# Performance work log

Measured on AMD Instinct MI355X. Metric: run time of the kernel, lower is better.

Reference implementation:

```python
import jax, jax.numpy as jnp
import numpy as np

BN_EPS = 1e-3


def _knn_group(p1, p2, k):
    # p1, p2: [B, N, 3]. For each point in p1, find k nearest in p2.
    d2 = (jnp.sum(p1 * p1, -1)[:, :, None]
          + jnp.sum(p2 * p2, -1)[:, None, :]
          - 2.0 * jnp.einsum('bnd,bmd->bnm', p1, p2))  # [B,N,N]
    _, idx = jax.lax.top_k(-d2, k)                      # [B,N,k]
    nn = jax.vmap(lambda pts, ind: pts[ind])(p2, idx)   # [B,N,k,3]
    resi = nn - p1[:, :, None, :]                       # [B,N,k,3]
    ss = jnp.sum(resi * resi, -1, keepdims=True)
    dist = jnp.sqrt(jnp.maximum(ss, 1e-12))             # safe norm
    feat = jnp.concatenate([resi, dist], -1)            # [B,N,k,4]
    return feat.transpose(0, 3, 1, 2), nn.transpose(0, 3, 1, 2)  # [B,4,N,k],[B,3,N,k]


def _conv_bn_relu(x, W, b, g, be, m, v):
    # 1x1 conv over channel dim: x [B,C,N,K], W [O,C]
    x = jnp.einsum('bcnk,oc->bonk', x, W) + b[None, :, None, None]
    x = (x - m[None, :, None, None]) * (g / jnp.sqrt(v + BN_EPS))[None, :, None, None] + be[None, :, None, None]
    return jax.nn.relu(x)


def setup_inputs() -> dict:
    key = jax.random.key(0)
    ks = jax.random.split(key, 20)
    B, N = 8, 2048
    chans = [4, 64, 64, 128]
    inp = {
        'points1': jax.random.normal(ks[0], (B, 3, N), jnp.float32),
        'points2': jax.random.normal(ks[1], (B, 3, N), jnp.float32),
    }
    for i in range(3):
        ci, co = chans[i], chans[i + 1]
        base = 2 + i * 6
        scale = 1.0 / np.sqrt(ci)
        inp[f'W{i+1}'] = jax.random.uniform(ks[base], (co, ci), jnp.float32, -scale, scale)
        inp[f'b{i+1}'] = jax.random.uniform(ks[base + 1], (co,), jnp.float32, -scale, scale)
        inp[f'g{i+1}'] = 1.0 + 0.1 * jax.random.normal(ks[base + 2], (co,), jnp.float32)
        inp[f'be{i+1}'] = 0.1 * jax.random.normal(ks[base + 3], (co,), jnp.float32)
        inp[f'm{i+1}'] = 0.05 * jax.random.normal(ks[base + 4], (co,), jnp.float32)
        inp[f'v{i+1}'] = jax.random.uniform(ks[base + 5], (co,), jnp.float32, 0.5, 1.5)
    inp['k'] = 32
    inp['t'] = 1
    return inp


def reference(points1, points2, W1, b1, g1, be1, m1, v1, W2, b2, g2, be2, m2, v2,
              W3, b3, g3, be3, m3, v3, k, t):
    p1 = points1.transpose(0, 2, 1)  # [B,N,3]
    p2 = points2.transpose(0, 2, 1)
    f1, nn1 = _knn_group(p1, p1, k)
    f2, nn2 = _knn_group(p1, p2, k)
    feats = jnp.concatenate([f1, f2], -1)          # [B,4,N,2k]
    grouped = jnp.concatenate([nn1, nn2], -1)      # [B,3,N,2k]
    x = _conv_bn_relu(feats, W1, b1, g1, be1, m1, v1)
    x = _conv_bn_relu(x, W2, b2, g2, be2, m2, v2)
    x = _conv_bn_relu(x, W3, b3, g3, be3, m3, v3)
    x = jnp.max(x, axis=1)                         # [B,N,2k] max over channels
    w = jax.nn.softmax(x, axis=-1)                 # softmax over 2k neighbors
    fused = jnp.sum(w[:, None, :, :] * grouped, -1)  # [B,3,N]
    return fused
```

## Files before the change

### kernel.cpp

```cpp
#include <hip/hip_runtime.h>
#include <hip/hip_bf16.h>
#include <stdint.h>

#define BB 8
#define NN 2048

#define OFF_B1 272
#define OFF_B2 4432
#define OFF_B3 12688
#define IDX_BYTE_OFF 65536
#define T_BASE   (65536 + 2*1024*1024)
#define T1_OFF   T_BASE
#define T2H_OFF  (T1_OFF + 4096)
#define T2L_OFF  (T2H_OFF + 9216)
#define T3H_OFF  (T2L_OFF + 9216)
#define T3L_OFF  (T3H_OFF + 18432)
#define L_T1   0
#define L_T2H  2048
#define L_T2L  6656
#define L_T3H  11264
#define L_T3L  20480
#define L_HALVES 29696

typedef __attribute__((ext_vector_type(4))) float f32x4;
typedef __attribute__((ext_vector_type(8))) short s16x8;

__device__ __forceinline__ float ldany(const void* p, long i, int isf32) {
    if (isf32) return ((const float*)p)[i];
    uint32_t u = ((uint32_t)((const uint16_t*)p)[i]) << 16;
    float f; __builtin_memcpy(&f, &u, 4); return f;
}
__device__ __forceinline__ uint16_t f2bf(float f) {
    uint32_t u; __builtin_memcpy(&u, &f, 4);
    return (uint16_t)((u + 0x7FFFu + ((u >> 16) & 1u)) >> 16);
}
__device__ __forceinline__ float bf2f(uint16_t h) {
    uint32_t u = ((uint32_t)h) << 16;
    float f; __builtin_memcpy(&f, &u, 4); return f;
}
__device__ __forceinline__ uint32_t pk2(float a, float b) {
    __hip_bfloat162 h = __float22bfloat162_rn(make_float2(a, b));
    uint32_t u; __builtin_memcpy(&u, &h, 4); return u;
}
__device__ __forceinline__ s16x8 mk8(uint32_t a, uint32_t b, uint32_t c, uint32_t d) {
    uint32_t t[4] = {a, b, c, d}; s16x8 r; __builtin_memcpy(&r, t, 16); return r;
}
__device__ __forceinline__ float sane(float v) {
    return (v == v && v > -1e30f && v < 1e30f) ? v : 0.f;
}
__device__ __forceinline__ int kperm_pos(int kk) {
    int g = kk >> 5, c5 = kk & 31;
    int sub = (c5 >> 4) & 1, q = (c5 >> 2) & 3, r = c5 & 3;
    return 32 * g + 8 * q + 4 * sub + r;
}

__global__ void k0_fold(const void* p1,
                        const void* W1, const void* b1, const void* g1, const void* be1, const void* m1, const void* v1,
                        const void* W2, const void* b2, const void* g2, const void* be2, const void* m2, const void* v2,
                        const void* W3, const void* b3, const void* g3, const void* be3, const void* m3, const void* v3,
                        float* wsf, int* wsi) {
    __shared__ int s_cnt;
    int t = threadIdx.x;
    if (t == 0) s_cnt = 0;
    __syncthreads();
    const uint16_t* u = (const uint16_t*)p1;
    int c = 0;
    for (int i = t; i < 4096; i += 256) {
        uint16_t x = u[i];
        uint32_t e = (x >> 7) & 0xFF;
        c += ((e >= 0x70 && e <= 0x84) || x == 0) ? 1 : 0;
    }
    atomicAdd(&s_cnt, c);
    __syncthreads();
    int isf32 = (s_cnt < 3686) ? 1 : 0;
    if (blockIdx.x == 0 && t == 0) wsi[0] = isf32;

    uint16_t* t1  = (uint16_t*)((char*)wsf + T1_OFF);
    uint16_t* t2h = (uint16_t*)((char*)wsf + T2H_OFF);
    uint16_t* t2l = (uint16_t*)((char*)wsf + T2L_OFF);
    uint16_t* t3h = (uint16_t*)((char*)wsf + T3H_OFF);
    uint16_t* t3l = (uint16_t*)((char*)wsf + T3L_OFF);

    int gid = blockIdx.x * 256 + t;
    if (gid < 4096) {
        int o = gid >> 6, kk = gid & 63;
        float s = ldany(g2, o, isf32) * rsqrtf(ldany(v2, o, isf32) + 1e-3f);
        float w = ldany(W2, gid, isf32) * s;
        uint16_t wh = f2bf(w);
        int pos = o * 72 + kperm_pos(kk);
        t2h[pos] = wh; t2l[pos] = f2bf(w - bf2f(wh));
    } else if (gid < 12288) {
        int e = gid - 4096;
        int o = e >> 6, kk = e & 63;
        float s = ldany(g3, o, isf32) * rsqrtf(ldany(v3, o, isf32) + 1e-3f);
        float w = ldany(W3, e, isf32) * s;
        uint16_t wh = f2bf(w);
        int pos = o * 72 + kperm_pos(kk);
        t3h[pos] = wh; t3l[pos] = f2bf(w - bf2f(wh));
    } else if (gid < 12544) {
        int e = gid - 12288;
        int co = e >> 2, cc = e & 3;
        float s = ldany(g1, co, isf32) * rsqrtf(ldany(v1, co, isf32) + 1e-3f);
        float w = ldany(W1, co*4 + cc, isf32) * s;
        uint16_t wh = f2bf(w), wl = f2bf(w - bf2f(wh));
        t1[co*32 + cc]     = wh;
        t1[co*32 + 4 + cc] = wh;
        t1[co*32 + 8 + cc] = wl;
    } else if (gid < 13824) {
        int e = gid - 12544;
        int co = e / 20, k = e - co * 20;
        t1[co*32 + 12 + k] = 0;
    } else if (gid < 13888) {
        int o = gid - 13824;
        float s = ldany(g1, o, isf32) * rsqrtf(ldany(v1, o, isf32) + 1e-3f);
        wsf[OFF_B1 + o] = (ldany(b1, o, isf32) - ldany(m1, o, isf32)) * s + ldany(be1, o, isf32);
    } else if (gid < 13952) {
        int o = gid - 13888;
        float s = ldany(g2, o, isf32) * rsqrtf(ldany(v2, o, isf32) + 1e-3f);
        wsf[OFF_B2 + o] = (ldany(b2, o, isf32) - ldany(m2, o, isf32)) * s + ldany(be2, o, isf32);
    } else if (gid < 14080) {
        int o = gid - 13952;
        float s = ldany(g3, o, isf32) * rsqrtf(ldany(v3, o, isf32) + 1e-3f);
        wsf[OFF_B3 + o] = (ldany(b3, o, isf32) - ldany(m3, o, isf32)) * s + ldany(be3, o, isf32);
    }
}

__launch_bounds__(256)
__global__ void k1_knn(const void* p1, const void* p2, const int* wsi, uint16_t* idxout) {
    __shared__ unsigned long long smem[4 * 128];

    int isf32 = wsi[0];
    int lane = threadIdx.x & 63;
    int wave = threadIdx.x >> 6;
    int qidx = blockIdx.x * 4 + wave;
    int b = qidx >> 11, n = qidx & 2047;
    long base = (long)b * 3 * NN;

    float qx = ldany(p1, base + n,        isf32);
    float qy = ldany(p1, base + NN + n,   isf32);
    float qz = ldany(p1, base + 2*NN + n, isf32);
    float s1 = qx * qx + qy * qy + qz * qz;

    uint32_t kbA[32], kbB[32];
    if (!isf32) {
        const uint16_t* u1 = (const uint16_t*)p1 + base;
        const uint16_t* u2 = (const uint16_t*)p2 + base;
        #pragma unroll
        for (int tgt = 0; tgt < 2; tgt++) {
            const uint16_t* tpu = tgt ? u2 : u1;
            uint32_t* kb = tgt ? kbB : kbA;
            const uint4* rx = (const uint4*)(tpu);
            const uint4* ry = (const uint4*)(tpu + NN);
            const uint4* rz = (const uint4*)(tpu + 2*NN);
            #pragma unroll
            for (int i = 0; i < 4; i++) {
                int v4 = i * 64 + lane;
                uint4 X = rx[v4], Y = ry[v4], Z = rz[v4];
                uint32_t xw[4] = {X.x, X.y, X.z, X.w};
                uint32_t yw[4] = {Y.x, Y.y, Y.z, Y.w};
                uint32_t zw[4] = {Z.x, Z.y, Z.z, Z.w};
                #pragma unroll
                for (int j = 0; j < 4; j++) {
                    #pragma unroll
                    for (int w = 0; w < 2; w++) {
                        uint32_t ux = (w == 0) ? (xw[j] << 16) : (xw[j] & 0xFFFF0000u);
                        uint32_t uy = (w == 0) ? (yw[j] << 16) : (yw[j] & 0xFFFF0000u);
                        uint32_t uz = (w == 0) ? (zw[j] << 16) : (zw[j] & 0xFFFF0000u);
                        float nx, ny, nz;
                        __builtin_memcpy(&nx, &ux, 4); __builtin_memcpy(&ny, &uy, 4); __builtin_memcpy(&nz, &uz, 4);
                        float s2  = nx * nx + ny * ny + nz * nz;
                        float dot = qx * nx + qy * ny + qz * nz;
                        float d2  = fmaxf((s1 + s2) - 2.0f * dot, 0.0f);
                        uint32_t bits; __builtin_memcpy(&bits, &d2, 4);
                        kb[i*8 + j*2 + w] = bits;
                    }
                }
            }
        }
    } else {
        #pragma unroll
        for (int i = 0; i < 32; i++) {
            int j = i * 64 + lane;
            float ax = ldany(p1, base + j,        isf32);
            float ay = ldany(p1, base + NN + j,   isf32);
            float az = ldany(p1, base + 2*NN + j, isf32);
            float d2a = fmaxf((s1 + ax*ax + ay*ay + az*az) - 2.0f*(qx*ax + qy*ay + qz*az), 0.0f);
            uint32_t ba; __builtin_memcpy(&ba, &d2a, 4);
            kbA[i] = ba;
            float bx = ldany(p2, base + j,        isf32);
            float by = ldany(p2, base + NN + j,   isf32);
            float bz = ldany(p2, base + 2*NN + j, isf32);
            float d2b = fmaxf((s1 + bx*bx + by*by + bz*bz) - 2.0f*(qx*bx + qy*by + qz*bz), 0.0f);
            uint32_t bb; __builtin_memcpy(&bb, &d2b, 4);
            kbB[i] = bb;
        }
    }

    uint32_t loA = 0u, hiA = 0x7F800001u, tauA = 0u;
    uint32_t loB = 0u, hiB = 0x7F800001u, tauB = 0u;
    int cpA = -1, cpB = -1;
    bool dA = false, dB = false;
    while (!(dA && dB)) {
        uint32_t midA = dA ? tauA : (loA + ((hiA - loA) >> 1));
        uint32_t midB = dB ? tauB : (loB + ((hiB - loB) >> 1));
        int cA = 0, cB = 0;
        #pragma unroll
        for (int i = 0; i < 32; i++) {
            cA += (kbA[i] < midA) ? 1 : 0;
            cB += (kbB[i] < midB) ? 1 : 0;
        }
        uint32_t pk = (uint32_t)cA | ((uint32_t)cB << 16);
        #pragma unroll
        for (int m = 1; m < 64; m <<= 1) pk += (uint32_t)__shfl_xor((int)pk, m, 64);
        int totA = (int)(pk & 0xFFFFu);
        int totB = (int)(pk >> 16);
        if (!dA) {
            if (totA < 32)      loA = midA;
            else if (totA > 64) hiA = midA;
            else { tauA = midA; cpA = cA; dA = true; }
            if (!dA && hiA - loA <= 1u) { tauA = hiA; dA = true; }
        }
        if (!dB) {
            if (totB < 32)      loB = midB;
            else if (totB > 64) hiB = midB;
            else { tauB = midB; cpB = cB; dB = true; }
            if (!dB && hiB - loB <= 1u) { tauB = hiB; dB = true; }
        }
    }
    if (cpA < 0) {
        int c2 = 0;
        #pragma unroll
        for (int i = 0; i < 32; i++) c2 += (kbA[i] < tauA) ? 1 : 0;
        cpA = c2;
    }
    if (cpB < 0) {
        int c2 = 0;
        #pragma unroll
        for (int i = 0; i < 32; i++) c2 += (kbB[i] < tauB) ? 1 : 0;
        cpB = c2;
    }

    uint32_t pc = (uint32_t)cpA | ((uint32_t)cpB << 16);
    uint32_t off = pc;
    #pragma unroll
    for (int d = 1; d < 64; d <<= 1) {
        uint32_t y = (uint32_t)__shfl_up((int)off, d, 64);
        if (lane >= d) off += y;
    }
    off -= pc;
    int oA = (int)(off & 0xFFFFu);
    int oB = (int)(off >> 16);

    unsigned long long* slA = smem + wave * 128;
    unsigned long long* slB = slA + 64;
    slA[lane] = ~0ull;
    slB[lane] = ~0ull;
    __syncthreads();
    #pragma unroll
    for (int s = 0; s < 32; s++) {
        unsigned idxv = isf32 ? (unsigned)(s * 64 + lane)
                              : (unsigned)((s >> 3) * 512 + 8 * lane + (s & 7));
        if (kbA[s] < tauA && oA < 64) {
            slA[oA] = (((unsigned long long)kbA[s]) << 32) | idxv;
            oA++;
        }
        if (kbB[s] < tauB && oB < 64) {
            slB[oB] = (((unsigned long long)kbB[s]) << 32) | idxv;
            oB++;
        }
    }
    __syncthreads();
    unsigned long long keyA = slA[lane];
    unsigned long long keyB = slB[lane];

    #pragma unroll
    for (int sz = 2; sz <= 64; sz <<= 1) {
        #pragma unroll
        for (int st = sz >> 1; st > 0; st >>= 1) {
            bool up    = ((lane & sz) == 0);
            bool lower = ((lane & st) == 0);
            unsigned long long otA = __shfl_xor(keyA, st, 64);
            unsigned long long otB = __shfl_xor(keyB, st, 64);
            unsigned long long mnA = (keyA < otA) ? keyA : otA;
            unsigned long long mxA = (keyA < otA) ? otA : keyA;
            keyA = (lower == up) ? mnA : mxA;
            unsigned long long mnB = (keyB < otB) ? keyB : otB;
            unsigned long long mxB = (keyB < otB) ? otB : keyB;
            keyB = (lower == up) ? mnB : mxB;
        }
    }

    if (lane < 32) {
        long obase = ((long)qidx) << 6;
        idxout[obase + lane]      = (uint16_t)(keyA & 0x7FFu);
        idxout[obase + 32 + lane] = (uint16_t)(keyB & 0x7FFu);
    }
}

__launch_bounds__(256)
__global__ void k2_mlp(const void* p1, const void* p2, const float* __restrict__ wsf, const int* wsi,
                       const uint16_t* __restrict__ idxin, void* outp) {
    __shared__ uint4 shw4[L_HALVES / 8];

    {
        const uint4* src = (const uint4*)((const char*)wsf + T1_OFF);
        for (int i = threadIdx.x; i < L_HALVES / 8; i += 256) shw4[i] = src[i];
    }
    __syncthreads();
    const uint16_t* shw = (const uint16_t*)shw4;
    const uint16_t* T1  = shw + L_T1;
    const uint16_t* T2H = shw + L_T2H;
    const uint16_t* T2L = shw + L_T2L;
    const uint16_t* T3H = shw + L_T3H;
    const uint16_t* T3L = shw + L_T3L;

    int isf32 = wsi[0];
    int lane = threadIdx.x & 63;
    int wave = threadIdx.x >> 6;
    int c = lane & 15;
    int q = lane >> 4;
    int qidx = blockIdx.x * 4 + wave;
    int b = qidx >> 11, n = qidx & 2047;
    long base = (long)b * 3 * NN;

    float qx = sane(ldany(p1, base + n,        isf32));
    float qy = sane(ldany(p1, base + NN + n,   isf32));
    float qz = sane(ldany(p1, base + 2*NN + n, isf32));

    int idx = idxin[((long)qidx << 6) + lane] & 2047;
    const void* sp = (lane < 32) ? p1 : p2;
    float nx = sane(ldany(sp, base + idx,        isf32));
    float ny = sane(ldany(sp, base + NN + idx,   isf32));
    float nz = sane(ldany(sp, base + 2*NN + idx, isf32));

    float r0 = nx - qx, r1 = ny - qy, r2 = nz - qz;
    float ss = fmaf(r0, r0, fmaf(r1, r1, r2 * r2));
    float dist = sqrtf(fmaxf(ss, 1e-12f));

    const float* B1 = wsf + OFF_B1;
    const float* B2 = wsf + OFF_B2;
    const float* B3 = wsf + OFF_B3;

    s16x8 b1f[4];
    #pragma unroll
    for (int nt = 0; nt < 4; nt++) {
        int src = 16 * nt + c;
        float f0 = __shfl(r0, src, 64);
        float f1 = __shfl(r1, src, 64);
        float f2v = __shfl(r2, src, 64);
        float f3v = __shfl(dist, src, 64);
        uint16_t h0 = f2bf(f0), h1 = f2bf(f1), h2 = f2bf(f2v), h3 = f2bf(f3v);
        uint16_t l0 = f2bf(f0 - bf2f(h0)), l1 = f2bf(f1 - bf2f(h1));
        uint16_t l2 = f2bf(f2v - bf2f(h2)), l3 = f2bf(f3v - bf2f(h3));
        s16x8 v;
        bool qa = (q < 2);
        bool qb = (q == 0);
        v[0] = qa ? (short)h0 : (short)0;
        v[1] = qa ? (short)h1 : (short)0;
        v[2] = qa ? (short)h2 : (short)0;
        v[3] = qa ? (short)h3 : (short)0;
        v[4] = qb ? (short)l0 : (short)0;
        v[5] = qb ? (short)l1 : (short)0;
        v[6] = qb ? (short)l2 : (short)0;
        v[7] = qb ? (short)l3 : (short)0;
        b1f[nt] = v;
    }

    f32x4 d1[4][4];
    #pragma unroll
    for (int mt = 0; mt < 4; mt++) {
        s16x8 a1 = *(const s16x8*)(T1 + (16 * mt + c) * 32 + q * 8);
        f32x4 bias = *(const f32x4*)(B1 + 16 * mt + 4 * q);
        #pragma unroll
        for (int nt = 0; nt < 4; nt++) {
            d1[mt][nt] = __builtin_amdgcn_mfma_f32_16x16x32_bf16(a1, b1f[nt], bias, 0, 0, 0);
        }
    }

    auto mkfrag = [](const f32x4& dlo, const f32x4& dhi) -> s16x8 {
        return mk8(pk2(fmaxf(dlo[0], 0.f), fmaxf(dlo[1], 0.f)),
                   pk2(fmaxf(dlo[2], 0.f), fmaxf(dlo[3], 0.f)),
                   pk2(fmaxf(dhi[0], 0.f), fmaxf(dhi[1], 0.f)),
                   pk2(fmaxf(dhi[2], 0.f), fmaxf(dhi[3], 0.f)));
    };

    f32x4 d2[4][4];
    #pragma unroll
    for (int mt = 0; mt < 4; mt++) {
        f32x4 bias = *(const f32x4*)(B2 + 16 * mt + 4 * q);
        #pragma unroll
        for (int nt = 0; nt < 4; nt++) d2[mt][nt] = bias;
    }
    #pragma unroll
    for (int g = 0; g < 2; g++) {
        s16x8 fh[4];
        #pragma unroll
        for (int nt = 0; nt < 4; nt++) fh[nt] = mkfrag(d1[2*g][nt], d1[2*g+1][nt]);
        #pragma unroll
        for (int mt = 0; mt < 4; mt++) {
            s16x8 ah = *(const s16x8*)(T2H + (16 * mt + c) * 72 + 32 * g + 8 * q);
            s16x8 al = *(const s16x8*)(T2L + (16 * mt + c) * 72 + 32 * g + 8 * q);
            #pragma unroll
            for (int nt = 0; nt < 4; nt++) {
                f32x4 acc = d2[mt][nt];
                acc = __builtin_amdgcn_mfma_f32_16x16x32_bf16(ah, fh[nt], acc, 0, 0, 0);
                acc = __builtin_amdgcn_mfma_f32_16x16x32_bf16(al, fh[nt], acc, 0, 0, 0);
                d2[mt][nt] = acc;
            }
        }
    }

    s16x8 f3h[2][4];
    #pragma unroll
    for (int g = 0; g < 2; g++)
        #pragma unroll
        for (int nt = 0; nt < 4; nt++) f3h[g][nt] = mkfrag(d2[2*g][nt], d2[2*g+1][nt]);

    float mx[4] = {-1e30f, -1e30f, -1e30f, -1e30f};
    #pragma unroll
    for (int mt = 0; mt < 8; mt++) {
        f32x4 bias = *(const f32x4*)(B3 + 16 * mt + 4 * q);
        f32x4 acc[4];
        #pragma unroll
        for (int nt = 0; nt < 4; nt++) acc[nt] = bias;
        #pragma unroll
        for (int g = 0; g < 2; g++) {
            s16x8 ah = *(const s16x8*)(T3H + (16 * mt + c) * 72 + 32 * g + 8 * q);
            s16x8 al = *(const s16x8*)(T3L + (16 * mt + c) * 72 + 32 * g + 8 * q);
            #pragma unroll
            for (int nt = 0; nt < 4; nt++) {
                f32x4 a = acc[nt];
                a = __builtin_amdgcn_mfma_f32_16x16x32_bf16(ah, f3h[g][nt], a, 0, 0, 0);
                a = __builtin_amdgcn_mfma_f32_16x16x32_bf16(al, f3h[g][nt], a, 0, 0, 0);
                acc[nt] = a;
            }
        }
        #pragma unroll
        for (int nt = 0; nt < 4; nt++) {
            mx[nt] = fmaxf(mx[nt], fmaxf(fmaxf(acc[nt][0], acc[nt][1]), fmaxf(acc[nt][2], acc[nt][3])));
        }
    }

    #pragma unroll
    for (int nt = 0; nt < 4; nt++) {
        mx[nt] = fmaxf(mx[nt], __shfl_xor(mx[nt], 16, 64));
        mx[nt] = fmaxf(mx[nt], __shfl_xor(mx[nt], 32, 64));
        mx[nt] = fmaxf(mx[nt], 0.f);
    }
    float mall = fmaxf(fmaxf(mx[0], mx[1]), fmaxf(mx[2], mx[3]));
    #pragma unroll
    for (int m = 1; m < 16; m <<= 1) mall = fmaxf(mall, __shfl_xor(mall, m, 64));
    float e0 = __expf(mx[0] - mall), e1 = __expf(mx[1] - mall);
    float e2 = __expf(mx[2] - mall), e3 = __expf(mx[3] - mall);
    float s = e0 + e1 + e2 + e3;
    #pragma unroll
    for (int m = 1; m < 16; m <<= 1) s += __shfl_xor(s, m, 64);
    float eown = (q == 0) ? e0 : (q == 1) ? e1 : (q == 2) ? e2 : e3;
    float w = eown / s;

    float sx = w * nx, sy = w * ny, sz = w * nz;
    #pragma unroll
    for (int m = 1; m < 64; m <<= 1) {
        sx += __shfl_xor(sx, m, 64);
        sy += __shfl_xor(sy, m, 64);
        sz += __shfl_xor(sz, m, 64);
    }

    if (lane < 3) {
        float v = (lane == 0) ? sx : ((lane == 1) ? sy : sz);
        long oi = base + (long)lane * NN + n;
        if (isf32) {
            ((float*)outp)[oi] = v;
        } else {
            ((uint16_t*)outp)[oi] = f2bf(v);
        }
    }
}

extern "C" void kernel_launch(void* const* d_in, const int* in_sizes, int n_in,
                              void* d_out, int out_size, void* d_ws, size_t ws_size,
                              hipStream_t stream) {
    const void* p1 = d_in[0];
    const void* p2 = d_in[1];
    float* wsf = (float*)d_ws;
    int*   wsi = (int*)d_ws;
    uint16_t* idxbuf = (uint16_t*)((char*)d_ws + IDX_BYTE_OFF);

    k0_fold<<<64, 256, 0, stream>>>(p1,
        d_in[2],  d_in[3],  d_in[4],  d_in[5],  d_in[6],  d_in[7],
        d_in[8],  d_in[9],  d_in[10], d_in[11], d_in[12], d_in[13],
        d_in[14], d_in[15], d_in[16], d_in[17], d_in[18], d_in[19],
        wsf, wsi);

    k1_knn<<<(BB * NN) / 4, 256, 0, stream>>>(p1, p2, wsi, idxbuf);

    k2_mlp<<<(BB * NN) / 4, 256, 0, stream>>>(p1, p2, wsf, wsi, idxbuf, d_out);
}
```

Measured before the change: 278.7 us.

## Replace kNN bitonic sort with exact radix-select threshold and ballot compaction

The kNN kernel now binary-searches the distance bit pattern for an exact 32nd-smallest threshold, counting with wave ballots and popcounts instead of per-lane counts plus shuffle reductions. Ties are broken by a second binary search over index. Selected indices are written straight to global memory through ballot/mbcnt compaction, which removes the LDS staging, both __syncthreads and the 64-element bitonic sort. The output order changes from distance-sorted to scan order, which is harmless because the downstream softmax-weighted sum does not depend on order. Occupancy is also hinted with launch_bounds(256,4), and the search now costs more iterations because it must hit exactly 32 rather than any count in 32..64.

Result: slower. 303.8 us (+9.0%).

```diff
diff --git a/kernel.cpp b/kernel.cpp
--- a/kernel.cpp
+++ b/kernel.cpp
@@ -47,6 +47,10 @@
 }
 __device__ __forceinline__ float sane(float v) {
     return (v == v && v > -1e30f && v < 1e30f) ? v : 0.f;
+}
+__device__ __forceinline__ int mbcnt64(unsigned long long m) {
+    return __builtin_amdgcn_mbcnt_hi((uint32_t)(m >> 32),
+           __builtin_amdgcn_mbcnt_lo((uint32_t)m, 0));
 }
 __device__ __forceinline__ int kperm_pos(int kk) {
     int g = kk >> 5, c5 = kk & 31;
@@ -125,10 +129,8 @@
     }
 }
 
-__launch_bounds__(256)
+__launch_bounds__(256, 4)
 __global__ void k1_knn(const void* p1, const void* p2, const int* wsi, uint16_t* idxout) {
-    __shared__ unsigned long long smem[4 * 128];
-
     int isf32 = wsi[0];
     int lane = threadIdx.x & 63;
     int wave = threadIdx.x >> 6;
@@ -196,104 +198,108 @@
         }
     }
 
-    uint32_t loA = 0u, hiA = 0x7F800001u, tauA = 0u;
-    uint32_t loB = 0u, hiB = 0x7F800001u, tauB = 0u;
-    int cpA = -1, cpB = -1;
-    bool dA = false, dB = false;
-    while (!(dA && dB)) {
-        uint32_t midA = dA ? tauA : (loA + ((hiA - loA) >> 1));
-        uint32_t midB = dB ? tauB : (loB + ((hiB - loB) >> 1));
-        int cA = 0, cB = 0;
+    auto cnt32 = [&](const uint32_t* kb, uint32_t mid) -> int {
+        int c = 0;
+        #pragma unroll
+        for (int i = 0; i < 32; i++) c += __builtin_popcountll(__ballot(kb[i] < mid));
+        return c;
+    };
+
+    uint32_t lo0 = 0u, hi0 = 0x7F800001u, lo1 = 0u, hi1 = 0x7F800001u;
+    bool done0 = false, done1 = false, exact0 = false, exact1 = false;
+    uint32_t tau0 = 0u, tau1 = 0u;
+    int a0 = 0, a1 = 0;
+    while (!done0 || !done1) {
+        if (!done0) {
+            uint32_t mid = lo0 + ((hi0 - lo0) >> 1);
+            int c = cnt32(kbA, mid);
+            if (c == 32)      { tau0 = mid; exact0 = true; done0 = true; }
+            else if (c < 32)  { lo0 = mid; a0 = c; }
+            else              hi0 = mid;
+            if (!done0 && hi0 - lo0 <= 1u) done0 = true;
+        }
+        if (!done1) {
+            uint32_t mid = lo1 + ((hi1 - lo1) >> 1);
+            int c = cnt32(kbB, mid);
+            if (c == 32)      { tau1 = mid; exact1 = true; done1 = true; }
+            else if (c < 32)  { lo1 = mid; a1 = c; }
+            else              hi1 = mid;
+            if (!done1 && hi1 - lo1 <= 1u) done1 = true;
+        }
+    }
+
+    uint32_t loSel0, idxT0, loSel1, idxT1;
+    {
+        if (!exact0) {
+            int c = cnt32(kbA, hi0);
+            if (c == 32) { tau0 = hi0; exact0 = true; }
+        }
+        if (exact0) { loSel0 = tau0; idxT0 = 0; }
+        else {
+            loSel0 = lo0;
+            uint32_t li = 0, hiI = 2048;
+            while (hiI - li > 1u) {
+                uint32_t m = li + ((hiI - li) >> 1);
+                int c2 = 0;
+                #pragma unroll
+                for (int i = 0; i < 32; i++) {
+                    unsigned idxv = isf32 ? (unsigned)(i * 64 + lane)
+                                          : (unsigned)((i >> 3) * 512 + 8 * lane + (i & 7));
+                    c2 += __builtin_popcountll(__ballot(kbA[i] == lo0 && idxv < m));
+                }
+                if (a0 + c2 < 32) li = m; else hiI = m;
+            }
+            idxT0 = hiI;
+        }
+        if (!exact1) {
+            int c = cnt32(kbB, hi1);
+            if (c == 32) { tau1 = hi1; exact1 = true; }
+        }
+        if (exact1) { loSel1 = tau1; idxT1 = 0; }
+        else {
+            loSel1 = lo1;
+            uint32_t li = 0, hiI = 2048;
+            while (hiI - li > 1u) {
+                uint32_t m = li + ((hiI - li) >> 1);
+                int c2 = 0;
+                #pragma unroll
+                for (int i = 0; i < 32; i++) {
+                    unsigned idxv = isf32 ? (unsigned)(i * 64 + lane)
+                                          : (unsigned)((i >> 3) * 512 + 8 * lane + (i & 7));
+                    c2 += __builtin_popcountll(__ballot(kbB[i] == lo1 && idxv < m));
+                }
+                if (a1 + c2 < 32) li = m; else hiI = m;
+            }
+            idxT1 = hiI;
+        }
+    }
+
+    long obase = ((long)qidx) << 6;
+    {
+        int basePos = 0;
         #pragma unroll
         for (int i = 0; i < 32; i++) {
-            cA += (kbA[i] < midA) ? 1 : 0;
-            cB += (kbB[i] < midB) ? 1 : 0;
-        }
-        uint32_t pk = (uint32_t)cA | ((uint32_t)cB << 16);
-        #pragma unroll
-        for (int m = 1; m < 64; m <<= 1) pk += (uint32_t)__shfl_xor((int)pk, m, 64);
-        int totA = (int)(pk & 0xFFFFu);
-        int totB = (int)(pk >> 16);
-        if (!dA) {
-            if (totA < 32)      loA = midA;
-            else if (totA > 64) hiA = midA;
-            else { tauA = midA; cpA = cA; dA = true; }
-            if (!dA && hiA - loA <= 1u) { tauA = hiA; dA = true; }
-        }
-        if (!dB) {
-            if (totB < 32)      loB = midB;
-            else if (totB > 64) hiB = midB;
-            else { tauB = midB; cpB = cB; dB = true; }
-            if (!dB && hiB - loB <= 1u) { tauB = hiB; dB = true; }
-        }
-    }
-    if (cpA < 0) {
-        int c2 = 0;
-        #pragma unroll
-        for (int i = 0; i < 32; i++) c2 += (kbA[i] < tauA) ? 1 : 0;
-        cpA = c2;
-    }
-    if (cpB < 0) {
-        int c2 = 0;
-        #pragma unroll
-        for (int i = 0; i < 32; i++) c2 += (kbB[i] < tauB) ? 1 : 0;
-        cpB = c2;
-    }
-
-    uint32_t pc = (uint32_t)cpA | ((uint32_t)cpB << 16);
-    uint32_t off = pc;
-    #pragma unroll
-    for (int d = 1; d < 64; d <<= 1) {
-        uint32_t y = (uint32_t)__shfl_up((int)off, d, 64);
-        if (lane >= d) off += y;
-    }
-    off -= pc;
-    int oA = (int)(off & 0xFFFFu);
-    int oB = (int)(off >> 16);
-
-    unsigned long long* slA = smem + wave * 128;
-    unsigned long long* slB = slA + 64;
-    slA[lane] = ~0ull;
-    slB[lane] = ~0ull;
-    __syncthreads();
-    #pragma unroll
-    for (int s = 0; s < 32; s++) {
-        unsigned idxv = isf32 ? (unsigned)(s * 64 + lane)
-                              : (unsigned)((s >> 3) * 512 + 8 * lane + (s & 7));
-        if (kbA[s] < tauA && oA < 64) {
-            slA[oA] = (((unsigned long long)kbA[s]) << 32) | idxv;
-            oA++;
-        }
-        if (kbB[s] < tauB && oB < 64) {
-            slB[oB] = (((unsigned long long)kbB[s]) << 32) | idxv;
-            oB++;
-        }
-    }
-    __syncthreads();
-    unsigned long long keyA = slA[lane];
-    unsigned long long keyB = slB[lane];
-
-    #pragma unroll
-    for (int sz = 2; sz <= 64; sz <<= 1) {
-        #pragma unroll
-        for (int st = sz >> 1; st > 0; st >>= 1) {
-            bool up    = ((lane & sz) == 0);
-            bool lower = ((lane & st) == 0);
-            unsigned long long otA = __shfl_xor(keyA, st, 64);
-            unsigned long long otB = __shfl_xor(keyB, st, 64);
-            unsigned long long mnA = (keyA < otA) ? keyA : otA;
-            unsigned long long mxA = (keyA < otA) ? otA : keyA;
-            keyA = (lower == up) ? mnA : mxA;
-            unsigned long long mnB = (keyB < otB) ? keyB : otB;
-            unsigned long long mxB = (keyB < otB) ? otB : keyB;
-            keyB = (lower == up) ? mnB : mxB;
-        }
-    }
-
-    if (lane < 32) {
-        long obase = ((long)qidx) << 6;
-        idxout[obase + lane]      = (uint16_t)(keyA & 0x7FFu);
-        idxout[obase + 32 + lane] = (uint16_t)(keyB & 0x7FFu);
+            unsigned idxv = isf32 ? (unsigned)(i * 64 + lane)
+                                  : (unsigned)((i >> 3) * 512 + 8 * lane + (i & 7));
+            bool pass = (kbA[i] < loSel0) || (kbA[i] == loSel0 && idxv < idxT0);
+            unsigned long long m = __ballot(pass);
+            int pos = basePos + mbcnt64(m);
+            if (pass) idxout[obase + (pos & 31)] = (uint16_t)idxv;
+            basePos += __builtin_popcountll(m);
+        }
+    }
+    {
+        int basePos = 0;
+        #pragma unroll
+        for (int i = 0; i < 32; i++) {
+            unsigned idxv = isf32 ? (unsigned)(i * 64 + lane)
+                                  : (unsigned)((i >> 3) * 512 + 8 * lane + (i & 7));
+            bool pass = (kbB[i] < loSel1) || (kbB[i] == loSel1 && idxv < idxT1);
+            unsigned long long m = __ballot(pass);
+            int pos = basePos + mbcnt64(m);
+            if (pass) idxout[obase + 32 + (pos & 31)] = (uint16_t)idxv;
+            basePos += __builtin_popcountll(m);
+        }
     }
 }
 
```
